# Performance work log

Measured on AMD Instinct MI355X. Metric: run time of the kernel, lower is better.

Reference implementation:

```python
import jax, jax.numpy as jnp
import numpy as np

N_USERS = 50000
N_ITEMS = 30000
N_ENTITIES = 100000
N_RELATIONS = 50
N_EDGES = 1500000
N_INTER = 1000000
D = 64
GAMMA = 0.1
MAX_ITER = 3


def _seg_sum(x, idx, n):
    return jax.ops.segment_sum(x, idx, num_segments=n)


def _seg_mean(x, idx, n):
    s = _seg_sum(x, idx, n)
    c = _seg_sum(jnp.ones((x.shape[0], 1), x.dtype), idx, n)
    return s / jnp.clip(c, 1.0)


def _masked_seg_mean(x, mask, idx, n):
    # scatter_mean over the subset of rows where mask is True (zeros for empty segments)
    w = mask.astype(x.dtype)[:, None]
    s = _seg_sum(x * w, idx, n)
    c = _seg_sum(w, idx, n)
    return s / jnp.clip(c, 1.0)


def _seg_softmax(p, idx, n):
    m = jax.ops.segment_max(p, idx, num_segments=n)
    e = jnp.exp(p - m[idx])
    z = _seg_sum(e, idx, n)
    return e / z[idx]


def _leaky_relu(x):
    return jnp.where(x >= 0, x, 0.01 * x)


def _normalize(x, eps=1e-12):
    n = jnp.linalg.norm(x, axis=1, keepdims=True)
    return x / jnp.maximum(n, eps)


def setup_inputs() -> dict:
    key = jax.random.key(0)
    ks = jax.random.split(key, 12)
    entity_emb = jax.random.normal(ks[0], (N_ENTITIES, D), jnp.float32) * 0.1
    user_emb = jax.random.normal(ks[1], (N_USERS, D), jnp.float32) * 0.1
    user_emb_cf = jax.random.normal(ks[2], (N_USERS, D), jnp.float32) * 0.1
    item_emb_cf = jax.random.normal(ks[3], (N_ITEMS, D), jnp.float32) * 0.1
    relation_weight = jax.random.normal(ks[4], (N_RELATIONS, D), jnp.float32) * 0.1
    edge_index = jax.random.randint(ks[5], (2, N_EDGES), 0, N_ENTITIES, jnp.int64 if jax.config.jax_enable_x64 else jnp.int32)
    edge_type = jax.random.randint(ks[6], (N_EDGES,), 0, N_RELATIONS, edge_index.dtype)
    rows = jax.random.randint(ks[7], (N_INTER, 1), 0, N_USERS, edge_index.dtype)
    cols = jax.random.randint(ks[8], (N_INTER, 1), 0, N_ITEMS, edge_index.dtype)
    interact_mat = jnp.concatenate([rows, cols], axis=1)
    W1_w = jax.random.normal(ks[9], (D, D), jnp.float32) * 0.1
    W1_b = jnp.zeros((D,), jnp.float32)
    W2_w = jax.random.normal(ks[10], (D, D), jnp.float32) * 0.1
    W2_b = jnp.zeros((D,), jnp.float32)
    return {
        "entity_emb": entity_emb, "user_emb": user_emb, "user_emb_cf": user_emb_cf,
        "item_emb_cf": item_emb_cf, "relation_weight": relation_weight,
        "W1_w": W1_w, "W1_b": W1_b, "W2_w": W2_w, "W2_b": W2_b,
        "edge_index": edge_index, "edge_type": edge_type, "interact_mat": interact_mat,
    }


def reference(entity_emb, user_emb, user_emb_cf, item_emb_cf, relation_weight,
              W1_w, W1_b, W2_w, W2_b, edge_index, edge_type, interact_mat):
    head, tail = edge_index[0], edge_index[1]
    cross = (head < N_ITEMS) ^ (tail < N_ITEMS)
    same = ~cross

    rel_emb = relation_weight[edge_type]          # [E, D]
    tail_emb = entity_emb[tail]                   # [E, D]

    agg1 = _masked_seg_mean(tail_emb * rel_emb, cross, head, N_ENTITIES)
    agg1 = _leaky_relu(agg1 @ W1_w.T + W1_b) / 2
    agg2 = _masked_seg_mean(tail_emb + rel_emb, same, head, N_ENTITIES)
    agg2 = _leaky_relu(agg2 @ W2_w.T + W2_b) / 2
    entity_agg = agg1 + agg2
    rel_ = _seg_mean(rel_emb, head, N_ENTITIES)   # [n_entities, D]

    mat_row = interact_mat[:, 0]
    mat_col = interact_mat[:, 1]
    item_emb_kg = entity_emb[:N_ITEMS]
    rel_i = rel_[:N_ITEMS]

    u, ucf, mask = None, None, None
    for i in range(MAX_ITER):
        ue = user_emb if u is None else u
        ucfe = user_emb_cf if ucf is None else ucf
        p = jax.nn.sigmoid(jnp.sum(ue[mat_row] * rel_i[mat_col] * item_emb_kg[mat_col], axis=1))
        pcf = jax.nn.sigmoid(jnp.sum(ucfe[mat_row] * item_emb_cf[mat_col], axis=1))
        p = _seg_softmax(p, mat_row, N_USERS)
        pcf = _seg_softmax(pcf, mat_row, N_USERS)
        mask = (jnp.abs(jax.nn.sigmoid(p) - jax.nn.sigmoid(pcf)) < GAMMA).astype(jnp.int32)[:, None]
        mf = mask.astype(p.dtype)
        u = _seg_sum(item_emb_kg[mat_col] * p[:, None] * mf, mat_row, N_USERS)
        ucf = _seg_sum(item_emb_cf[mat_col] * pcf[:, None] * mf, mat_row, N_USERS)
        if i < MAX_ITER - 1:
            u = _normalize(u)
            ucf = _normalize(ucf)

    item_agg = _seg_mean(user_emb_cf[mat_row], mat_col, N_ITEMS)
    return entity_agg, u, ucf, item_agg, mask
```

## Files before the change

kernel.cpp:

```cpp
#include <hip/hip_runtime.h>

#define NU 50000
#define NI 30000
#define NE 100000
#define NEDGE 1500000
#define NINTER 1000000
#define GAMMA 0.1f
#define CAP 192
#define KR 5
#define KSTG (4 * KR)
#define SB 1024

__device__ __forceinline__ float frcp(float x) { return __builtin_amdgcn_rcpf(x); }
__device__ __forceinline__ float fsgm(float x) { return frcp(1.0f + __expf(-x)); }
__device__ __forceinline__ float dot4(float4 a, float4 b) {
  return a.x * b.x + a.y * b.y + a.z * b.z + a.w * b.w;
}
__device__ __forceinline__ int gidx(const void* p, long long i, int is64) {
  return is64 ? (int)((const long long*)p)[i] : ((const int*)p)[i];
}

__global__ void k_detect(const int* __restrict__ ei32, int* __restrict__ flag) {
  int all_zero = 1;
  for (int i = 1; i < 64; i += 2)
    if (ei32[i] != 0) { all_zero = 0; break; }
  *flag = all_zero;
}

__global__ void k_hist(const void* __restrict__ ei, const void* __restrict__ im,
                       int* __restrict__ cntE, int* __restrict__ cntR,
                       int* __restrict__ cntC, const int* __restrict__ flagp) {
  int t = blockIdx.x * blockDim.x + threadIdx.x;
  int f = *flagp;
  if (t < NEDGE) atomicAdd(&cntE[gidx(ei, t, f)], 1);
  if (t < NINTER) {
    atomicAdd(&cntR[gidx(im, 2LL * t, f)], 1);
    atomicAdd(&cntC[gidx(im, 2LL * t + 1, f)], 1);
  }
}

__global__ void k_scan1(const int* __restrict__ in, int* __restrict__ out,
                        int* __restrict__ part, int n) {
  __shared__ int tmp[SB];
  int g = blockIdx.x * SB + threadIdx.x;
  int v = (g < n) ? in[g] : 0;
  tmp[threadIdx.x] = v; __syncthreads();
  for (int off = 1; off < SB; off <<= 1) {
    int t = (threadIdx.x >= off) ? tmp[threadIdx.x - off] : 0;
    __syncthreads();
    tmp[threadIdx.x] += t;
    __syncthreads();
  }
  if (g < n) out[g] = tmp[threadIdx.x] - v;
  if (threadIdx.x == SB - 1) part[blockIdx.x] = tmp[threadIdx.x];
}

__global__ void k_scan2(int* __restrict__ part, int nb) {
  __shared__ int tmp[SB];
  int v = (threadIdx.x < nb) ? part[threadIdx.x] : 0;
  tmp[threadIdx.x] = v; __syncthreads();
  for (int off = 1; off < SB; off <<= 1) {
    int t = (threadIdx.x >= off) ? tmp[threadIdx.x - off] : 0;
    __syncthreads();
    tmp[threadIdx.x] += t;
    __syncthreads();
  }
  if (threadIdx.x < nb) part[threadIdx.x] = tmp[threadIdx.x] - v;
}

__global__ void k_scan3(int* __restrict__ out, const int* __restrict__ part, int n) {
  int g = blockIdx.x * SB + threadIdx.x;
  if (g < n) out[g] += part[blockIdx.x];
}

__global__ void k_scat(const void* __restrict__ ei, const void* __restrict__ et,
                       const void* __restrict__ im,
                       const int* __restrict__ startE, int* __restrict__ curE, int* __restrict__ SE,
                       const int* __restrict__ startR, int* __restrict__ curR,
                       int* __restrict__ SIcol, int* __restrict__ SIorig,
                       const int* __restrict__ startC, int* __restrict__ curC,
                       int* __restrict__ SCrow, const int* __restrict__ flagp) {
  int t = blockIdx.x * blockDim.x + threadIdx.x;
  int f = *flagp;
  if (t < NEDGE) {
    int h = gidx(ei, t, f), tl = gidx(ei, NEDGE + t, f), r = gidx(et, t, f);
    int pos = startE[h] + atomicAdd(&curE[h], 1);
    ((int2*)SE)[pos] = make_int2(tl, r);
  }
  if (t < NINTER) {
    int r = gidx(im, 2LL * t, f), c = gidx(im, 2LL * t + 1, f);
    int pr = startR[r] + atomicAdd(&curR[r], 1);
    SIcol[pr] = c; SIorig[pr] = t;
    int pc = startC[c] + atomicAdd(&curC[c], 1);
    SCrow[pc] = r;
  }
}

__global__ __launch_bounds__(256) void k_aggE(
    const int* __restrict__ SE, const int* __restrict__ startE, const int* __restrict__ cntE,
    const float* __restrict__ ent, const float* __restrict__ relw,
    const float* __restrict__ W1w, const float* __restrict__ W1b,
    const float* __restrict__ W2w, const float* __restrict__ W2b,
    float* __restrict__ out_entity, float* __restrict__ RIE) {
  __shared__ float w1[64 * 65], w2[64 * 65], b1[64], b2[64];
  __shared__ float xs1[4][64], xs2[4][64], xs3[4][64];
  int tid = threadIdx.x;
  for (int i = tid; i < 4096; i += 256) {
    w1[(i >> 6) * 65 + (i & 63)] = W1w[i];
    w2[(i >> 6) * 65 + (i & 63)] = W2w[i];
  }
  if (tid < 64) { b1[tid] = W1b[tid]; b2[tid] = W2b[tid]; }
  __syncthreads();
  int w = tid >> 6, lane = tid & 63;
  int g = lane >> 4, q = lane & 15;
  int h = blockIdx.x * 4 + w;
  if (h >= NE) return;
  int s = startE[h], n = cntE[h];
  bool hI = (h < NI);
  float4 a1 = {0, 0, 0, 0}, a2 = {0, 0, 0, 0}, rs = {0, 0, 0, 0};
  int c1 = 0;
  for (int i0 = 0; i0 < n; i0 += 4) {
    int i = i0 + g;
    bool act = i < n;
    if (act) {
      int2 tr = ((const int2*)SE)[s + i];
      const float4 te = *(const float4*)&ent[tr.x * 64 + 4 * q];
      const float4 re = *(const float4*)&relw[tr.y * 64 + 4 * q];
      rs.x += re.x; rs.y += re.y; rs.z += re.z; rs.w += re.w;
      if (hI != (tr.x < NI)) {
        a1.x += te.x * re.x; a1.y += te.y * re.y;
        a1.z += te.z * re.z; a1.w += te.w * re.w;
        c1++;
      } else {
        a2.x += te.x + re.x; a2.y += te.y + re.y;
        a2.z += te.z + re.z; a2.w += te.w + re.w;
      }
    }
  }
#pragma unroll
  for (int off = 16; off <= 32; off <<= 1) {
    a1.x += __shfl_xor(a1.x, off, 64); a1.y += __shfl_xor(a1.y, off, 64);
    a1.z += __shfl_xor(a1.z, off, 64); a1.w += __shfl_xor(a1.w, off, 64);
    a2.x += __shfl_xor(a2.x, off, 64); a2.y += __shfl_xor(a2.y, off, 64);
    a2.z += __shfl_xor(a2.z, off, 64); a2.w += __shfl_xor(a2.w, off, 64);
    rs.x += __shfl_xor(rs.x, off, 64); rs.y += __shfl_xor(rs.y, off, 64);
    rs.z += __shfl_xor(rs.z, off, 64); rs.w += __shfl_xor(rs.w, off, 64);
    c1 += __shfl_xor(c1, off, 64);
  }
  int c2 = n - c1;
  float r1 = frcp((float)max(c1, 1)), r2 = frcp((float)max(c2, 1));
  float rn = frcp((float)max(n, 1));
  if (g == 0) {
    *(float4*)&xs1[w][4 * q] = make_float4(a1.x * r1, a1.y * r1, a1.z * r1, a1.w * r1);
    *(float4*)&xs2[w][4 * q] = make_float4(a2.x * r2, a2.y * r2, a2.z * r2, a2.w * r2);
    *(float4*)&xs3[w][4 * q] = make_float4(rs.x * rn, rs.y * rn, rs.z * rn, rs.w * rn);
  }
  __asm__ volatile("s_waitcnt lgkmcnt(0)");
  int d = lane;
  float acc1 = b1[d], acc2 = b2[d];
#pragma unroll 8
  for (int k = 0; k < 64; k++) {
    acc1 += xs1[w][k] * w1[d * 65 + k];
    acc2 += xs2[w][k] * w2[d * 65 + k];
  }
  acc1 = (acc1 >= 0.f ? acc1 : 0.01f * acc1) * 0.5f;
  acc2 = (acc2 >= 0.f ? acc2 : 0.01f * acc2) * 0.5f;
  out_entity[h * 64 + d] = acc1 + acc2;
  if (hI) RIE[h * 64 + d] = xs3[w][d] * ent[h * 64 + d];
}

__global__ __launch_bounds__(256, 4) void k_phaseB(
    const int* __restrict__ SIcol, const int* __restrict__ SIorig,
    const int* __restrict__ startR, const int* __restrict__ cntR,
    const float* __restrict__ ue, const float* __restrict__ uce,
    const float* __restrict__ RIE, const float* __restrict__ ent,
    const float* __restrict__ icf,
    float* __restrict__ out_u, float* __restrict__ out_ucf,
    float* __restrict__ out_mask) {
  __shared__ float eP[4][CAP + 4], ePC[4][CAP + 4];
  __shared__ int cols[4][CAP + 4];
  int tid = threadIdx.x, w = tid >> 6, lane = tid & 63;
  int g = lane >> 4, q = lane & 15;
  int r = blockIdx.x * 4 + w;
  if (r >= NU) return;
  int s = startR[r], n = cntR[r];
  if (n > CAP) n = CAP;
  for (int i = lane; i < n; i += 64) cols[w][i] = SIcol[s + i];
  __asm__ volatile("s_waitcnt lgkmcnt(0) vmcnt(0)");
  float4 u4  = *(const float4*)&ue[r * 64 + 4 * q];
  float4 uc4 = *(const float4*)&uce[r * 64 + 4 * q];

  float4 rieS[KR], icfS[KR], entS[KR];
#pragma unroll
  for (int kk = 0; kk < KR; kk++) {
    int i = 4 * kk + g;
    rieS[kk] = make_float4(0, 0, 0, 0);
    icfS[kk] = make_float4(0, 0, 0, 0);
    entS[kk] = make_float4(0, 0, 0, 0);
    if (i < n) {
      int c = cols[w][i];
      rieS[kk] = *(const float4*)&RIE[c * 64 + 4 * q];
      icfS[kk] = *(const float4*)&icf[c * 64 + 4 * q];
      entS[kk] = *(const float4*)&ent[c * 64 + 4 * q];
    }
  }

  for (int it = 0; it < 3; it++) {
    float Zp = 0.f, ZCp = 0.f;
    float epS[KR], epcS[KR];
#pragma unroll
    for (int kk = 0; kk < KR; kk++) {
      int i = 4 * kk + g;
      bool act = i < n;
      float v1 = 0.f, v2 = 0.f;
      if (act) {
        v1 = dot4(u4,  rieS[kk]);
        v2 = dot4(uc4, icfS[kk]);
      }
#pragma unroll
      for (int off = 1; off <= 8; off <<= 1) {
        v1 += __shfl_xor(v1, off, 64);
        v2 += __shfl_xor(v2, off, 64);
      }
      float ep = __expf(fsgm(v1)), epc = __expf(fsgm(v2));
      epS[kk] = ep; epcS[kk] = epc;
      if (act) { Zp += ep; ZCp += epc; }
    }
    for (int i0 = KSTG; i0 < n; i0 += 4) {
      int i = i0 + g;
      bool act = i < n;
      float v1 = 0.f, v2 = 0.f;
      if (act) {
        int c = cols[w][i];
        v1 = dot4(u4,  *(const float4*)&RIE[c * 64 + 4 * q]);
        v2 = dot4(uc4, *(const float4*)&icf[c * 64 + 4 * q]);
      }
#pragma unroll
      for (int off = 1; off <= 8; off <<= 1) {
        v1 += __shfl_xor(v1, off, 64);
        v2 += __shfl_xor(v2, off, 64);
      }
      float ep = __expf(fsgm(v1)), epc = __expf(fsgm(v2));
      if (act) {
        if (q == 0) { eP[w][i] = ep; ePC[w][i] = epc; }
        Zp += ep; ZCp += epc;
      }
    }
    float Zs = Zp, ZCs = ZCp;
#pragma unroll
    for (int off = 16; off <= 32; off <<= 1) {
      Zs += __shfl_xor(Zs, off, 64);
      ZCs += __shfl_xor(ZCs, off, 64);
    }
    __asm__ volatile("s_waitcnt lgkmcnt(0)");
    float rz = frcp(Zs), rzc = frcp(ZCs);
    float4 ua = {0, 0, 0, 0}, uca = {0, 0, 0, 0};
#pragma unroll
    for (int kk = 0; kk < KR; kk++) {
      int i = 4 * kk + g;
      if (i < n) {
        float p = epS[kk] * rz, pc = epcS[kk] * rzc;
        bool m = fabsf(fsgm(p) - fsgm(pc)) < GAMMA;
        if (it == 2 && q == 0) out_mask[SIorig[s + i]] = m ? 1.0f : 0.0f;
        if (m) {
          ua.x += entS[kk].x * p; ua.y += entS[kk].y * p;
          ua.z += entS[kk].z * p; ua.w += entS[kk].w * p;
          uca.x += icfS[kk].x * pc; uca.y += icfS[kk].y * pc;
          uca.z += icfS[kk].z * pc; uca.w += icfS[kk].w * pc;
        }
      }
    }
    for (int i0 = KSTG; i0 < n; i0 += 4) {
      int i = i0 + g;
      if (i < n) {
        int c = cols[w][i];
        float p = eP[w][i] * rz, pc = ePC[w][i] * rzc;
        bool m = fabsf(fsgm(p) - fsgm(pc)) < GAMMA;
        if (it == 2 && q == 0) out_mask[SIorig[s + i]] = m ? 1.0f : 0.0f;
        if (m) {
          const float4 e4 = *(const float4*)&ent[c * 64 + 4 * q];
          const float4 i4 = *(const float4*)&icf[c * 64 + 4 * q];
          ua.x += e4.x * p; ua.y += e4.y * p; ua.z += e4.z * p; ua.w += e4.w * p;
          uca.x += i4.x * pc; uca.y += i4.y * pc; uca.z += i4.z * pc; uca.w += i4.w * pc;
        }
      }
    }
#pragma unroll
    for (int off = 16; off <= 32; off <<= 1) {
      ua.x += __shfl_xor(ua.x, off, 64); ua.y += __shfl_xor(ua.y, off, 64);
      ua.z += __shfl_xor(ua.z, off, 64); ua.w += __shfl_xor(ua.w, off, 64);
      uca.x += __shfl_xor(uca.x, off, 64); uca.y += __shfl_xor(uca.y, off, 64);
      uca.z += __shfl_xor(uca.z, off, 64); uca.w += __shfl_xor(uca.w, off, 64);
    }
    if (it < 2) {
      float s1 = dot4(ua, ua), s2 = dot4(uca, uca);
#pragma unroll
      for (int off = 1; off <= 8; off <<= 1) {
        s1 += __shfl_xor(s1, off, 64);
        s2 += __shfl_xor(s2, off, 64);
      }
      float k1 = frcp(fmaxf(sqrtf(s1), 1e-12f)), k2 = frcp(fmaxf(sqrtf(s2), 1e-12f));
      ua.x *= k1; ua.y *= k1; ua.z *= k1; ua.w *= k1;
      uca.x *= k2; uca.y *= k2; uca.z *= k2; uca.w *= k2;
    }
    u4 = ua; uc4 = uca;
  }
  if (g == 0) {
    *(float4*)&out_u[r * 64 + 4 * q] = u4;
    *(float4*)&out_ucf[r * 64 + 4 * q] = uc4;
  }
}

__global__ __launch_bounds__(256) void k_itemA(
    const int* __restrict__ SCrow, const int* __restrict__ startC,
    const int* __restrict__ cntC, const float* __restrict__ ucf,
    float* __restrict__ out_item) {
  int tid = threadIdx.x, w = tid >> 6, lane = tid & 63;
  int g = lane >> 4, q = lane & 15;
  int c = blockIdx.x * 4 + w;
  if (c >= NI) return;
  int s = startC[c], n = cntC[c];
  float4 a = {0, 0, 0, 0};
  for (int i0 = 0; i0 < n; i0 += 4) {
    int i = i0 + g;
    if (i < n) {
      const float4 v = *(const float4*)&ucf[SCrow[s + i] * 64 + 4 * q];
      a.x += v.x; a.y += v.y; a.z += v.z; a.w += v.w;
    }
  }
#pragma unroll
  for (int off = 16; off <= 32; off <<= 1) {
    a.x += __shfl_xor(a.x, off, 64); a.y += __shfl_xor(a.y, off, 64);
    a.z += __shfl_xor(a.z, off, 64); a.w += __shfl_xor(a.w, off, 64);
  }
  float rn = frcp((float)max(n, 1));
  if (g == 0) {
    *(float4*)&out_item[c * 64 + 4 * q] =
        make_float4(a.x * rn, a.y * rn, a.z * rn, a.w * rn);
  }
}

static void scan(int* cnt, int* start, int* part, int n, hipStream_t st) {
  int nb = (n + SB - 1) / SB;
  k_scan1<<<nb, SB, 0, st>>>(cnt, start, part, n);
  k_scan2<<<1, SB, 0, st>>>(part, nb);
  k_scan3<<<nb, SB, 0, st>>>(start, part, n);
}

extern "C" void kernel_launch(void* const* d_in, const int* in_sizes, int n_in,
                              void* d_out, int out_size, void* d_ws, size_t ws_size,
                              hipStream_t stream) {
  const float* entity_emb  = (const float*)d_in[0];
  const float* user_emb    = (const float*)d_in[1];
  const float* user_emb_cf = (const float*)d_in[2];
  const float* item_emb_cf = (const float*)d_in[3];
  const float* relw        = (const float*)d_in[4];
  const float* W1w = (const float*)d_in[5];
  const float* W1b = (const float*)d_in[6];
  const float* W2w = (const float*)d_in[7];
  const float* W2b = (const float*)d_in[8];
  const void* edge_index   = d_in[9];
  const void* edge_type    = d_in[10];
  const void* interact_mat = d_in[11];

  float* out = (float*)d_out;
  float* out_entity = out;
  float* out_u      = out + 6400000;
  float* out_ucf    = out + 9600000;
  float* out_item   = out + 12800000;
  float* out_mask   = out + 14720000;

  float* W = (float*)d_ws;
  int*   SE     = (int*)W;
  int*   SIcol  = (int*)(W + 3000000);
  int*   SIorig = (int*)(W + 4000000);
  int*   SCrow  = (int*)(W + 5000000);
  float* RIE    = W + 6000000;
  int*   cntE   = (int*)(W + 7920000);
  int*   startE = (int*)(W + 8020000);
  int*   curE   = (int*)(W + 8120000);
  int*   cntR   = (int*)(W + 8220000);
  int*   startR = (int*)(W + 8270000);
  int*   curR   = (int*)(W + 8320000);
  int*   cntC   = (int*)(W + 8370000);
  int*   startC = (int*)(W + 8400000);
  int*   curC   = (int*)(W + 8430000);
  int*   part   = (int*)(W + 8460000);
  int*   FL     = (int*)(W + 8462048);

  k_detect<<<1, 1, 0, stream>>>((const int*)edge_index, FL);
  hipMemsetAsync(cntE, 0, (size_t)(8462048 - 7920000) * 4, stream);

  int gb = (NEDGE + 255) / 256;
  k_hist<<<gb, 256, 0, stream>>>(edge_index, interact_mat, cntE, cntR, cntC, FL);
  scan(cntE, startE, part, NE, stream);
  scan(cntR, startR, part, NU, stream);
  scan(cntC, startC, part, NI, stream);
  k_scat<<<gb, 256, 0, stream>>>(edge_index, edge_type, interact_mat,
                                 startE, curE, SE,
                                 startR, curR, SIcol, SIorig,
                                 startC, curC, SCrow, FL);

  k_aggE<<<(NE + 3) / 4, 256, 0, stream>>>(SE, startE, cntE, entity_emb, relw,
                                           W1w, W1b, W2w, W2b, out_entity, RIE);
  k_phaseB<<<(NU + 3) / 4, 256, 0, stream>>>(SIcol, SIorig, startR, cntR,
                                             user_emb, user_emb_cf, RIE,
                                             entity_emb, item_emb_cf,
                                             out_u, out_ucf, out_mask);
  k_itemA<<<(NI + 3) / 4, 256, 0, stream>>>(SCrow, startC, cntC, user_emb_cf, out_item);
}
```

Baseline: 957.8 us.

## Stripe histogram and scatter atomics by key range across block cohorts

The histogram and scatter kernels now use 2048 blocks split into 8 cohorts. Each cohort scans all inputs but only does atomics and writes for keys in its own range (an eighth of the entity, user or item space). The goal is to keep each cohort's atomic and scatter targets in a smaller, cache-friendly region, perhaps local to one XCD. The edge record is also packed from an int2 into a single int (tail in 17 bits, relation above it), which halves SE traffic in the scatter and in aggE. In exchange, every cohort re-reads the full index arrays, so input reads grow eightfold, and the packing only holds while entity ids fit in 17 bits.

```diff
diff --git a/kernel.cpp b/kernel.cpp
--- a/kernel.cpp
+++ b/kernel.cpp
@@ -11,6 +11,11 @@
 #define KSTG (4 * KR)
 #define SB 1024
 
+#define STRIPE_E 12500
+#define STRIPE_R 6250
+#define STRIPE_C 3750
+#define SCATB 2048
+
 __device__ __forceinline__ float frcp(float x) { return __builtin_amdgcn_rcpf(x); }
 __device__ __forceinline__ float fsgm(float x) { return frcp(1.0f + __expf(-x)); }
 __device__ __forceinline__ float dot4(float4 a, float4 b) {
@@ -27,15 +32,26 @@
   *flag = all_zero;
 }
 
-__global__ void k_hist(const void* __restrict__ ei, const void* __restrict__ im,
-                       int* __restrict__ cntE, int* __restrict__ cntR,
-                       int* __restrict__ cntC, const int* __restrict__ flagp) {
-  int t = blockIdx.x * blockDim.x + threadIdx.x;
+__global__ __launch_bounds__(256) void k_hist(
+    const void* __restrict__ ei, const void* __restrict__ im,
+    int* __restrict__ cntE, int* __restrict__ cntR,
+    int* __restrict__ cntC, const int* __restrict__ flagp) {
   int f = *flagp;
-  if (t < NEDGE) atomicAdd(&cntE[gidx(ei, t, f)], 1);
-  if (t < NINTER) {
-    atomicAdd(&cntR[gidx(im, 2LL * t, f)], 1);
-    atomicAdd(&cntC[gidx(im, 2LL * t + 1, f)], 1);
+  int coh = blockIdx.x & 7;
+  int ct = (blockIdx.x >> 3) * 256 + threadIdx.x;
+  int cstride = (gridDim.x >> 3) * 256;
+  int loE = coh * STRIPE_E, hiE = loE + STRIPE_E;
+  int loR = coh * STRIPE_R, hiR = loR + STRIPE_R;
+  int loC = coh * STRIPE_C, hiC = loC + STRIPE_C;
+  for (int e = ct; e < NEDGE; e += cstride) {
+    int h = gidx(ei, e, f);
+    if (h >= loE && h < hiE) atomicAdd(&cntE[h], 1);
+  }
+  for (int t = ct; t < NINTER; t += cstride) {
+    int r = gidx(im, 2LL * t, f);
+    int c = gidx(im, 2LL * t + 1, f);
+    if (r >= loR && r < hiR) atomicAdd(&cntR[r], 1);
+    if (c >= loC && c < hiC) atomicAdd(&cntC[c], 1);
   }
 }
 
@@ -73,26 +89,40 @@
   if (g < n) out[g] += part[blockIdx.x];
 }
 
-__global__ void k_scat(const void* __restrict__ ei, const void* __restrict__ et,
-                       const void* __restrict__ im,
-                       const int* __restrict__ startE, int* __restrict__ curE, int* __restrict__ SE,
-                       const int* __restrict__ startR, int* __restrict__ curR,
-                       int* __restrict__ SIcol, int* __restrict__ SIorig,
-                       const int* __restrict__ startC, int* __restrict__ curC,
-                       int* __restrict__ SCrow, const int* __restrict__ flagp) {
-  int t = blockIdx.x * blockDim.x + threadIdx.x;
+__global__ __launch_bounds__(256) void k_scat(
+    const void* __restrict__ ei, const void* __restrict__ et,
+    const void* __restrict__ im,
+    const int* __restrict__ startE, int* __restrict__ curE, int* __restrict__ SE,
+    const int* __restrict__ startR, int* __restrict__ curR,
+    int* __restrict__ SIcol, int* __restrict__ SIorig,
+    const int* __restrict__ startC, int* __restrict__ curC,
+    int* __restrict__ SCrow, const int* __restrict__ flagp) {
   int f = *flagp;
-  if (t < NEDGE) {
-    int h = gidx(ei, t, f), tl = gidx(ei, NEDGE + t, f), r = gidx(et, t, f);
-    int pos = startE[h] + atomicAdd(&curE[h], 1);
-    ((int2*)SE)[pos] = make_int2(tl, r);
-  }
-  if (t < NINTER) {
-    int r = gidx(im, 2LL * t, f), c = gidx(im, 2LL * t + 1, f);
-    int pr = startR[r] + atomicAdd(&curR[r], 1);
-    SIcol[pr] = c; SIorig[pr] = t;
-    int pc = startC[c] + atomicAdd(&curC[c], 1);
-    SCrow[pc] = r;
+  int coh = blockIdx.x & 7;
+  int ct = (blockIdx.x >> 3) * 256 + threadIdx.x;
+  int cstride = (gridDim.x >> 3) * 256;
+  int loE = coh * STRIPE_E, hiE = loE + STRIPE_E;
+  int loR = coh * STRIPE_R, hiR = loR + STRIPE_R;
+  int loC = coh * STRIPE_C, hiC = loC + STRIPE_C;
+  for (int e = ct; e < NEDGE; e += cstride) {
+    int h = gidx(ei, e, f);
+    if (h >= loE && h < hiE) {
+      int tl = gidx(ei, NEDGE + (long long)e, f), r = gidx(et, e, f);
+      int pos = startE[h] + atomicAdd(&curE[h], 1);
+      SE[pos] = tl | (r << 17);
+    }
+  }
+  for (int t = ct; t < NINTER; t += cstride) {
+    int r = gidx(im, 2LL * t, f);
+    int c = gidx(im, 2LL * t + 1, f);
+    if (r >= loR && r < hiR) {
+      int pr = startR[r] + atomicAdd(&curR[r], 1);
+      SIcol[pr] = c; SIorig[pr] = t;
+    }
+    if (c >= loC && c < hiC) {
+      int pc = startC[c] + atomicAdd(&curC[c], 1);
+      SCrow[pc] = r;
+    }
   }
 }
 
@@ -123,11 +153,12 @@
     int i = i0 + g;
     bool act = i < n;
     if (act) {
-      int2 tr = ((const int2*)SE)[s + i];
-      const float4 te = *(const float4*)&ent[tr.x * 64 + 4 * q];
-      const float4 re = *(const float4*)&relw[tr.y * 64 + 4 * q];
+      int v = SE[s + i];
+      int tl = v & 0x1FFFF, rl = v >> 17;
+      const float4 te = *(const float4*)&ent[tl * 64 + 4 * q];
+      const float4 re = *(const float4*)&relw[rl * 64 + 4 * q];
       rs.x += re.x; rs.y += re.y; rs.z += re.z; rs.w += re.w;
-      if (hI != (tr.x < NI)) {
+      if (hI != (tl < NI)) {
         a1.x += te.x * re.x; a1.y += te.y * re.y;
         a1.z += te.z * re.z; a1.w += te.w * re.w;
         c1++;
@@ -391,15 +422,14 @@
   k_detect<<<1, 1, 0, stream>>>((const int*)edge_index, FL);
   hipMemsetAsync(cntE, 0, (size_t)(8462048 - 7920000) * 4, stream);
 
-  int gb = (NEDGE + 255) / 256;
-  k_hist<<<gb, 256, 0, stream>>>(edge_index, interact_mat, cntE, cntR, cntC, FL);
+  k_hist<<<SCATB, 256, 0, stream>>>(edge_index, interact_mat, cntE, cntR, cntC, FL);
   scan(cntE, startE, part, NE, stream);
   scan(cntR, startR, part, NU, stream);
   scan(cntC, startC, part, NI, stream);
-  k_scat<<<gb, 256, 0, stream>>>(edge_index, edge_type, interact_mat,
-                                 startE, curE, SE,
-                                 startR, curR, SIcol, SIorig,
-                                 startC, curC, SCrow, FL);
+  k_scat<<<SCATB, 256, 0, stream>>>(edge_index, edge_type, interact_mat,
+                                    startE, curE, SE,
+                                    startR, curR, SIcol, SIorig,
+                                    startC, curC, SCrow, FL);
 
   k_aggE<<<(NE + 3) / 4, 256, 0, stream>>>(SE, startE, cntE, entity_emb, relw,
                                            W1w, W1b, W2w, W2b, out_entity, RIE);
```

After: 900.8 us. -6.0%, faster.
